# Optimization experiments

Hardware: AMD Instinct MI355X
Metric: run time of the kernel (lower is better)

## Reference

```python
import jax, jax.numpy as jnp
import numpy as np
import math

B, S, F, D = 8, 2048, 1024, 1024
NEG = -1e9


def setup_inputs() -> dict:
    key = jax.random.key(0)
    ks = jax.random.split(key, 5)
    x = jax.random.normal(ks[0], (B, S, F), dtype=jnp.float32)
    r_mat = jax.random.normal(ks[1], (B, S, S), dtype=jnp.float32)
    # shared causal attention mask [S, S] (1 = keep, 0 = masked)
    attn_mask = jnp.tril(jnp.ones((S, S), dtype=jnp.float32))
    # per-batch padding mask [B, 1, S]: last 128 tokens of half the batch padded
    pad = jnp.ones((B, 1, S), dtype=jnp.float32)
    pad = pad.at[B // 2:, :, S - 128:].set(0.0)
    Wq = jax.random.normal(ks[2], (F, D), dtype=jnp.float32) / math.sqrt(F)
    Wk = jax.random.normal(ks[3], (F, D), dtype=jnp.float32) / math.sqrt(F)
    Wv = jax.random.normal(ks[4], (F, D), dtype=jnp.float32) / math.sqrt(F)
    return {"x": x, "r_mat": r_mat, "attn_mask": attn_mask, "pad_mask": pad,
            "Wq": Wq, "Wk": Wk, "Wv": Wv}


def reference(x, r_mat, attn_mask, pad_mask, Wq, Wk, Wv):
    scale = math.sqrt(x.shape[-1])  # original scales by sqrt(features)
    q = jnp.einsum('bsf,fd->bsd', x, Wq)
    k = jnp.einsum('bsf,fd->bsd', x, Wk)
    v = jnp.einsum('bsf,fd->bsd', x, Wv)
    scores = jnp.einsum('bsd,btd->bst', q, k) / scale  # [B, S, S]
    keep = (pad_mask != 0.0) & (attn_mask[None] != 0.0)  # [B, S, S] broadcast
    r = jnp.where(keep, r_mat, NEG)
    r = jax.nn.softmax(r, axis=-1)
    scores = jnp.where(keep, scores + r, NEG)
    prob = jax.nn.softmax(scores, axis=-1)
    return jnp.einsum('bst,btd->bsd', prob, v)
```

## Files before the change

kernel.cpp:

```cpp
#include <hip/hip_runtime.h>
#include <hip/hip_bf16.h>

#define B_ 8
#define S_ 2048
#define F_ 1024
#define D_ 1024
#define TRI_ 136
#define TELEM_ 16384

typedef unsigned short u16;
typedef float f32x4 __attribute__((ext_vector_type(4)));
typedef __bf16 bf16x8 __attribute__((ext_vector_type(8)));
typedef unsigned short u16x8 __attribute__((ext_vector_type(8)));

__device__ __forceinline__ u16 f2bf(float f) {
  union { float f; unsigned u; } v; v.f = f;
  unsigned r = v.u + 0x7fff + ((v.u >> 16) & 1);
  return (u16)(r >> 16);
}
__device__ __forceinline__ float bf2f(u16 b) {
  union { unsigned u; float f; } v; v.u = ((unsigned)b) << 16;
  return v.f;
}

__device__ __forceinline__ void stage16(const u16* g, u16* l) {
  __builtin_amdgcn_global_load_lds(
      (const __attribute__((address_space(1))) void*)g,
      (__attribute__((address_space(3))) void*)l, 16, 0, 0);
}

__device__ __forceinline__ int xcd_swz(int f, int n) {
  int per = n >> 3;
  return (f & 7) * per + (f >> 3);
}


__global__ __launch_bounds__(256) void prep(const float* __restrict__ x,
                                            const float* __restrict__ Wq,
                                            const float* __restrict__ Wk,
                                            const float* __restrict__ Wv,
                                            u16* __restrict__ xb,
                                            u16* __restrict__ Wt) {
  __shared__ float tile[32][33];
  if (blockIdx.x < 2048) {
    int n4 = (B_ * S_ * F_) / 4;
    for (int i = blockIdx.x * 256 + threadIdx.x; i < n4; i += 2048 * 256) {
      float4 v = ((const float4*)x)[i];
      ushort4 o;
      o.x = f2bf(v.x); o.y = f2bf(v.y); o.z = f2bf(v.z); o.w = f2bf(v.w);
      ((ushort4*)xb)[i] = o;
    }
  } else {
    int f = blockIdx.x - 2048;
    int z = f >> 10;
    int f2 = f & 1023;
    int f0 = (f2 >> 5) * 32, d0 = (f2 & 31) * 32;
    const float* W = (z == 0) ? Wq : ((z == 1) ? Wk : Wv);
    int tx = threadIdx.x & 31, ty = threadIdx.x >> 5;
    for (int i = 0; i < 4; i++)
      tile[ty + i * 8][tx] = W[(size_t)(f0 + ty + i * 8) * D_ + d0 + tx];
    __syncthreads();
    u16* o = Wt + (size_t)z * D_ * F_;
    for (int i = 0; i < 4; i++)
      o[(size_t)(d0 + ty + i * 8) * F_ + f0 + tx] = f2bf(tile[tx][ty + i * 8]);
  }
}

__global__ __launch_bounds__(256) void er_pass(const float* __restrict__ r,
                                               const float* __restrict__ pm,
                                               u16* __restrict__ er,
                                               float* __restrict__ rowsum) {
  int row = blockIdx.x;
  int b = row >> 11, s = row & 2047;
  if (threadIdx.x == 0) rowsum[row] = 0.f;
  const float4* rp = (const float4*)(r + (size_t)row * S_);
  const float4* pp = (const float4*)(pm + (size_t)b * S_);
  int nk = (s >> 2) + 1;
  int nw = ((s >> 7) + 1) << 5;
  float4 ev[8];
  float acc = 0.f;
  #pragma unroll
  for (int it = 0; it < 8; it++) {
    int i = threadIdx.x + it * 256;
    if (i < nk) {
      float4 rv = rp[i], pv = pp[i];
      int t0 = i << 2;
      float4 e;
      #pragma unroll
      for (int j = 0; j < 4; j++) {
        bool keep = (t0 + j <= s) && ((&pv.x)[j] != 0.f);
        (&e.x)[j] = keep ? __expf((&rv.x)[j] - 16.f) : 0.f;
        acc += (&e.x)[j];
      }
      ev[it] = e;
    }
  }
  for (int off = 1; off < 64; off <<= 1) acc += __shfl_xor(acc, off);
  __shared__ float wsum[4];
  int lane = threadIdx.x & 63, w = threadIdx.x >> 6;
  if (lane == 0) wsum[w] = acc;
  __syncthreads();
  float invr = 1.f / (wsum[0] + wsum[1] + wsum[2] + wsum[3]);
  int c = s >> 7, rin = s & 127;
  u16* tb = er + (size_t)(b * TRI_ + c * (c + 1) / 2) * TELEM_ + rin * 128;
  #pragma unroll
  for (int it = 0; it < 8; it++) {
    int i = threadIdx.x + it * 256;
    if (i < nw) {
      int t0 = i << 2;
      float4 pv = pp[i];
      ushort4 o;
      #pragma unroll
      for (int j = 0; j < 4; j++) {
        bool keep = (t0 + j <= s) && ((&pv.x)[j] != 0.f);
        float val = keep ? (&ev[it].x)[j] * invr : -1e9f;
        (&o.x)[j] = f2bf(val);
      }
      *(ushort4*)(tb + (size_t)(t0 >> 7) * TELEM_ + (t0 & 127)) = o;
    }
  }
}

__global__ __launch_bounds__(256) void r_rowsum(const float* __restrict__ r,
                                                const float* __restrict__ pm,
                                                float* __restrict__ rs) {
  int row = blockIdx.x;
  int b = row >> 11, s = row & 2047;
  const float4* rp = (const float4*)(r + (size_t)row * S_);
  const float4* pp = (const float4*)(pm + (size_t)b * S_);
  int nv = (s >> 2) + 1;
  float acc = 0.f;
  for (int i = threadIdx.x; i < nv; i += 256) {
    float4 rv = rp[i];
    float4 pv = pp[i];
    int t0 = i << 2;
    #pragma unroll
    for (int j = 0; j < 4; j++) {
      int t = t0 + j;
      if (t <= s && (&pv.x)[j] != 0.f) acc += __expf((&rv.x)[j] - 16.f);
    }
  }
  for (int off = 1; off < 64; off <<= 1) acc += __shfl_xor(acc, off);
  __shared__ float wsum[4];
  int lane = threadIdx.x & 63, w = threadIdx.x >> 6;
  if (lane == 0) wsum[w] = acc;
  __syncthreads();
  if (threadIdx.x == 0) rs[row] = wsum[0] + wsum[1] + wsum[2] + wsum[3];
}


__device__ __forceinline__ bf16x8 readfrag(const u16* lds, int row, int ks, int hi) {
  int c = ((ks << 6) + (hi << 4)) ^ ((row & 7) << 4);
  return *(const bf16x8*)((const char*)lds + row * 128 + c);
}

#define SYNC_POINT()                                                             \
  __builtin_amdgcn_sched_barrier(0);                                             \
  __builtin_amdgcn_s_barrier();                                                  \
  __builtin_amdgcn_sched_barrier(0);


__device__ __forceinline__ void stageA(const u16* __restrict__ src, int ld, int h,
                                       u16* ldsA, int w, int l) {
  int base = ((w >> 2) * 128) + h * 64 + ((w & 3) * 16);
  int r = l >> 3, ch = (l & 7) ^ (l >> 3);
  #pragma unroll
  for (int i = 0; i < 2; i++) {
    int row = base + i * 8;
    stage16(src + (size_t)(row + r) * ld + ch * 8, ldsA + row * 64);
  }
}
__device__ __forceinline__ void stageB(const u16* __restrict__ src, int ld, int h,
                                       u16* ldsB, int w, int l) {
  int base = h * 128 + w * 16;
  int r = l >> 3, ch = (l & 7) ^ (l >> 3);
  #pragma unroll
  for (int i = 0; i < 2; i++) {
    int row = base + i * 8;
    stage16(src + (size_t)(row + r) * ld + ch * 8, ldsB + row * 64);
  }
}

#define MFMAQ(AF, KB, MB)                                                        \
  __builtin_amdgcn_s_setprio(1);                                                 \
  _Pragma("unroll")                                                              \
  for (int m = 0; m < 4; m++)                                                    \
    _Pragma("unroll")                                                            \
    for (int n = 0; n < 4; n++)                                                  \
      acc[(MB) + m][n] = __builtin_amdgcn_mfma_f32_16x16x32_bf16(                \
          AF[m], bfr[(KB) + n], acc[(MB) + m][n], 0, 0, 0);                      \
  __builtin_amdgcn_s_setprio(0);

__device__ __forceinline__ void gemm256(const u16* __restrict__ A, int lda,
                                        const u16* __restrict__ B, int ldb,
                                        int nT, u16* lds, f32x4 acc[8][4]) {
  const int t = threadIdx.x, w = t >> 6, l = t & 63;
  const int wr = w >> 2, wc = w & 3;
  u16* A0 = lds;           u16* B0 = lds + 16384;
  u16* A1 = lds + 32768;   u16* B1 = lds + 49152;

  #pragma unroll
  for (int m = 0; m < 8; m++)
    #pragma unroll
    for (int n = 0; n < 4; n++)
      #pragma unroll
      for (int j = 0; j < 4; j++) acc[m][n][j] = 0.f;

  stageB(B, ldb, 0, B0, w, l);
  stageB(B, ldb, 1, B0, w, l);
  stageA(A, lda, 0, A0, w, l);
  stageA(A, lda, 1, A0, w, l);
  if (nT > 1) stageA(A + 64, lda, 0, A1, w, l);
  asm volatile("s_waitcnt vmcnt(4)" ::: "memory");
  SYNC_POINT()

  const int arow = wr * 128 + (l & 15), hi = l >> 4;
  const int brow = wc * 64 + (l & 15);

  for (int kt = 0; kt < nT; kt++) {
    u16* cA = (kt & 1) ? A1 : A0;
    u16* cB = (kt & 1) ? B1 : B0;
    u16* nA = (kt & 1) ? A0 : A1;
    u16* nB = (kt & 1) ? B0 : B1;
    const u16* An1 = A + (size_t)(kt + 1) * 64;
    const u16* Bn1 = B + (size_t)(kt + 1) * 64;
    const u16* An2 = A + (size_t)(kt + 2) * 64;
    const bool has1 = (kt + 1 < nT), has2 = (kt + 2 < nT);
    bf16x8 af0[4], af1[4], bfr[8];

    #pragma unroll
    for (int m = 0; m < 4; m++) af0[m] = readfrag(cA, arow + m * 16, 0, hi);
    #pragma unroll
    for (int n = 0; n < 4; n++) bfr[n] = readfrag(cB, brow + n * 16, 0, hi);
    #pragma unroll
    for (int m = 0; m < 4; m++) af1[m] = readfrag(cA, arow + m * 16, 1, hi);
    #pragma unroll
    for (int n = 0; n < 4; n++) bfr[4 + n] = readfrag(cB, brow + n * 16, 1, hi);
    if (has1) stageB(Bn1, ldb, 0, nB, w, l);
    MFMAQ(af0, 0, 0)

    if (has1) {
      stageB(Bn1, ldb, 1, nB, w, l);
      asm volatile("s_waitcnt vmcnt(4)" ::: "memory");
    } else {
      asm volatile("s_waitcnt vmcnt(0)" ::: "memory");
    }
    SYNC_POINT()
    MFMAQ(af1, 4, 0)

    #pragma unroll
    for (int m = 0; m < 4; m++) af0[m] = readfrag(cA, arow + 64 + m * 16, 0, hi);
    #pragma unroll
    for (int m = 0; m < 4; m++) af1[m] = readfrag(cA, arow + 64 + m * 16, 1, hi);
    if (has2) stageA(An2, lda, 0, cA, w, l);
    MFMAQ(af0, 0, 4)

    if (has1) stageA(An1, lda, 1, nA, w, l);
    if (has1 && has2)  { asm volatile("s_waitcnt vmcnt(4)" ::: "memory"); }
    else if (has1)     { asm volatile("s_waitcnt vmcnt(2)" ::: "memory"); }
    else               { asm volatile("s_waitcnt vmcnt(0)" ::: "memory"); }
    SYNC_POINT()
    MFMAQ(af1, 4, 4)
  }
}

__device__ __forceinline__ void store256_bf16(f32x4 acc[8][4], u16* smem,
                                              u16* dst, int ld) {
  int t = threadIdx.x, w = t >> 6, l = t & 63;
  int wr = w >> 2, wc = w & 3;
  #pragma unroll
  for (int q = 0; q < 4; q++) {
    __syncthreads();
    if (wr == (q >> 1)) {
      int mb = (q & 1) * 4;
      #pragma unroll
      for (int mm = 0; mm < 4; mm++)
        #pragma unroll
        for (int j = 0; j < 4; j++) {
          int row = mm * 16 + (l >> 4) * 4 + j;
          #pragma unroll
          for (int n = 0; n < 4; n++)
            smem[row * 264 + wc * 64 + n * 16 + (l & 15)] = f2bf(acc[mb + mm][n][j]);
        }
    }
    __syncthreads();
    #pragma unroll
    for (int i = 0; i < 4; i++) {
      int idx = i * 512 + t;
      int row = idx >> 5, ch = idx & 31;
      *(u16x8*)(dst + (size_t)(q * 64 + row) * ld + ch * 8) =
          *(const u16x8*)(smem + row * 264 + ch * 8);
    }
  }
}

__global__ __launch_bounds__(512, 2) void gemm_qkv(
    const u16* __restrict__ xb, const u16* __restrict__ Wt,
    u16* __restrict__ qb, u16* __restrict__ kb, u16* __restrict__ vT) {
  __shared__ __align__(16) u16 lds[65536];
  int z = blockIdx.z;
  f32x4 acc[8][4];
  if (z < 2) {
    int m0 = blockIdx.x * 256, n0 = blockIdx.y * 256;
    gemm256(xb + (size_t)m0 * F_, F_,
            Wt + (size_t)z * D_ * F_ + (size_t)n0 * F_, F_, F_ / 64, lds, acc);
    store256_bf16(acc, lds, ((z == 0) ? qb : kb) + (size_t)m0 * D_ + n0, D_);
  } else {
    int d0 = blockIdx.y * 256, s0g = blockIdx.x * 256;
    gemm256(Wt + 2ULL * D_ * F_ + (size_t)d0 * F_, F_,
            xb + (size_t)s0g * F_, F_, F_ / 64, lds, acc);
    int b = s0g >> 11, s0 = s0g & 2047;
    store256_bf16(acc, lds, vT + (size_t)b * D_ * S_ + (size_t)d0 * S_ + s0, S_);
  }
}


template <int PACKA>
__device__ __forceinline__ void gemm128(const u16* __restrict__ A, int lda,
                                        const u16* __restrict__ B, int ldb,
                                        int nT, u16* lds, f32x4 acc[4][4]) {
  const int t = threadIdx.x, w = t >> 6, l = t & 63;
  const int wr = w >> 1, wc = w & 1;
  u16* A0 = lds;          u16* B0 = lds + 8192;
  u16* A1 = lds + 16384;  u16* B1 = lds + 24576;

  auto asrc = [&](int kt) -> const u16* {
    return PACKA ? A + (size_t)(kt >> 1) * TELEM_ + (kt & 1) * 64
                 : A + (size_t)kt * 64;
  };

  #pragma unroll
  for (int m = 0; m < 4; m++)
    #pragma unroll
    for (int n = 0; n < 4; n++)
      #pragma unroll
      for (int j = 0; j < 4; j++) acc[m][n][j] = 0.f;

  auto stg = [&](const u16* src, int ld, int h, u16* dst) {
    int base = h * 64 + w * 16;
    int r = l >> 3, ch = (l & 7) ^ (l >> 3);
    #pragma unroll
    for (int i = 0; i < 2; i++) {
      int row = base + i * 8;
      stage16(src + (size_t)(row + r) * ld + ch * 8, dst + row * 64);
    }
  };

  stg(asrc(0), PACKA ? 128 : lda, 0, A0);
  stg(asrc(0), PACKA ? 128 : lda, 1, A0);
  stg(B, ldb, 0, B0);
  stg(B, ldb, 1, B0);
  if (nT > 1) {
    stg(asrc(1), PACKA ? 128 : lda, 0, A1);
    stg(asrc(1), PACKA ? 128 : lda, 1, A1);
    asm volatile("s_waitcnt vmcnt(4)" ::: "memory");
  } else {
    asm volatile("s_waitcnt vmcnt(0)" ::: "memory");
  }
  SYNC_POINT()

  const int arow = wr * 64 + (l & 15), brow = wc * 64 + (l & 15), hi = l >> 4;

  for (int kt = 0; kt < nT; kt++) {
    u16* cA = (kt & 1) ? A1 : A0;
    u16* cB = (kt & 1) ? B1 : B0;
    u16* nB = (kt & 1) ? B0 : B1;
    const bool has1 = (kt + 1 < nT), has2 = (kt + 2 < nT);
    bf16x8 a0f[4], b0f[4], a1f[4], b1f[4];

    #pragma unroll
    for (int m = 0; m < 4; m++) a0f[m] = readfrag(cA, arow + m * 16, 0, hi);
    #pragma unroll
    for (int n = 0; n < 4; n++) b0f[n] = readfrag(cB, brow + n * 16, 0, hi);
    #pragma unroll
    for (int m = 0; m < 4; m++) a1f[m] = readfrag(cA, arow + m * 16, 1, hi);
    #pragma unroll
    for (int n = 0; n < 4; n++) b1f[n] = readfrag(cB, brow + n * 16, 1, hi);
    if (has1) {
      stg(B + (size_t)(kt + 1) * 64, ldb, 0, nB);
      stg(B + (size_t)(kt + 1) * 64, ldb, 1, nB);
    }
    __builtin_amdgcn_s_setprio(1);
    #pragma unroll
    for (int m = 0; m < 4; m++)
      #pragma unroll
      for (int n = 0; n < 4; n++)
        acc[m][n] = __builtin_amdgcn_mfma_f32_16x16x32_bf16(a0f[m], b0f[n], acc[m][n], 0, 0, 0);
    __builtin_amdgcn_s_setprio(0);
    asm volatile("s_waitcnt lgkmcnt(0)" ::: "memory");
    SYNC_POINT()

    if (has2) {
      stg(asrc(kt + 2), PACKA ? 128 : lda, 0, cA);
      stg(asrc(kt + 2), PACKA ? 128 : lda, 1, cA);
    }
    __builtin_amdgcn_s_setprio(1);
    #pragma unroll
    for (int m = 0; m < 4; m++)
      #pragma unroll
      for (int n = 0; n < 4; n++)
        acc[m][n] = __builtin_amdgcn_mfma_f32_16x16x32_bf16(a1f[m], b1f[n], acc[m][n], 0, 0, 0);
    __builtin_amdgcn_s_setprio(0);
    if (has2)      { asm volatile("s_waitcnt vmcnt(4)" ::: "memory"); }
    else if (has1) { asm volatile("s_waitcnt vmcnt(0)" ::: "memory"); }
    SYNC_POINT()
  }
}

__device__ __forceinline__ void tri_decode(int x, int& mt, int& nt) {
  mt = (int)((sqrtf(8.f * x + 1.f) - 1.f) * 0.5f);
  while ((mt + 1) * (mt + 2) / 2 <= x) mt++;
  while (mt * (mt + 1) / 2 > x) mt--;
  nt = x - mt * (mt + 1) / 2;
}

__global__ __launch_bounds__(512, 2) void attn_scores_er(
    const u16* __restrict__ qb, const u16* __restrict__ kb,
    const u16* __restrict__ er, u16* __restrict__ P,
    float* __restrict__ rowsum) {
  __shared__ __align__(16) u16 lds[65536];
  int f = xcd_swz(blockIdx.x + 36 * blockIdx.y, 288);
  int x = f % 36, b = f / 36;
  int MT, NT; tri_decode(x, MT, NT);
  int m0 = MT * 256, n0 = NT * 256;
  f32x4 acc[8][4];
  gemm256(qb + ((size_t)b * S_ + m0) * D_, D_,
          kb + ((size_t)b * S_ + n0) * D_, D_, D_ / 64, lds, acc);
  int t = threadIdx.x, w = t >> 6, l = t & 63;
  int wr = w >> 2, wc = w & 3;
  float* fs = (float*)lds;
  const u16* erb = er + (size_t)b * TRI_ * TELEM_;
  u16* Pb = P + (size_t)b * TRI_ * TELEM_;
  #pragma unroll
  for (int q = 0; q < 4; q++) {
    __syncthreads();
    if (wr == (q >> 1)) {
      int mb = (q & 1) * 4;
      #pragma unroll
      for (int mm = 0; mm < 4; mm++)
        #pragma unroll
        for (int j = 0; j < 4; j++) {
          int row = mm * 16 + (l >> 4) * 4 + j;
          #pragma unroll
          for (int n = 0; n < 4; n++)
            fs[row * 260 + wc * 64 + n * 16 + (l & 15)] = acc[mb + mm][n][j];
        }
    }
    __syncthreads();
    int row = t >> 3, cg = t & 7;
    int rin256 = q * 64 + row;
    int mt128 = 2 * MT + (rin256 >> 7), rin128 = rin256 & 127;
    int nt128 = 2 * NT + (cg >> 2);
    bool valid = (nt128 <= mt128);
    float rsum = 0.f;
    if (valid) {
      size_t sb = (size_t)(mt128 * (mt128 + 1) / 2 + nt128) * TELEM_
                  + (size_t)rin128 * 128 + (cg & 3) * 32;
      const u16* et = erb + sb;
      u16* pt = Pb + sb;
      const float* fsc = fs + row * 260 + cg * 32;
      #pragma unroll
      for (int cc = 0; cc < 4; cc++) {
        int ch = (cg + cc) & 3;
        f32x4 q0 = *(const f32x4*)(fsc + ch * 8);
        f32x4 q1 = *(const f32x4*)(fsc + ch * 8 + 4);
        u16x8 e8 = *(const u16x8*)(et + ch * 8);
        u16x8 o;
        #pragma unroll
        for (int k = 0; k < 8; k++) {
          float qk = (k < 4) ? q0[k] : q1[k - 4];
          float e = __expf(fmaf(qk, 0.03125f, bf2f(e8[k]) - 16.f));
          u16 pb = f2bf(e); o[k] = pb; rsum += bf2f(pb);
        }
        *(u16x8*)(pt + ch * 8) = o;
      }
    }
    rsum += __shfl_xor(rsum, 1);
    rsum += __shfl_xor(rsum, 2);
    rsum += __shfl_xor(rsum, 4);
    if ((t & 7) == 0) atomicAdd(&rowsum[b * S_ + m0 + rin256], rsum);
  }
}

__global__ __launch_bounds__(256, 2) void attn_scores_rm(
    const u16* __restrict__ qb, const u16* __restrict__ kb,
    const float* __restrict__ r_mat, const float* __restrict__ pm,
    const float* __restrict__ rs_r, u16* __restrict__ P,
    float* __restrict__ rowsum) {
  __shared__ __align__(16) u16 lds[32768];
  int f = xcd_swz(blockIdx.x + 136 * blockIdx.y, 1088);
  int x = f % 136, b = f / 136;
  int mt, nt; tri_decode(x, mt, nt);
  int m0 = mt * 128, n0 = nt * 128;
  f32x4 acc[4][4];
  gemm128<0>(qb + ((size_t)b * S_ + m0) * D_, D_,
             kb + ((size_t)b * S_ + n0) * D_, D_, D_ / 64, lds, acc);
  int t = threadIdx.x, w = t >> 6, l = t & 63;
  int wr = w >> 1, wc = w & 1;
  float* fs = (float*)lds;
  const float* rb = r_mat + (size_t)b * S_ * S_;
  const float* pmp = pm + (size_t)b * S_ + n0;
  size_t tbase = (size_t)(b * TRI_ + mt * (mt + 1) / 2 + nt) * TELEM_;
  #pragma unroll
  for (int h = 0; h < 2; h++) {
    __syncthreads();
    if (wr == h) {
      #pragma unroll
      for (int m = 0; m < 4; m++)
        #pragma unroll
        for (int j = 0; j < 4; j++) {
          int row = m * 16 + (l >> 4) * 4 + j;
          #pragma unroll
          for (int n = 0; n < 4; n++)
            fs[row * 132 + wc * 64 + n * 16 + (l & 15)] = acc[m][n][j];
        }
    }
    __syncthreads();
    int row = t >> 2, cg = t & 3;
    int srow = m0 + h * 64 + row;
    float invr = 1.f / rs_r[b * S_ + srow];
    const float* rrow = rb + (size_t)srow * S_ + n0 + cg * 32;
    u16* pt = P + tbase + (size_t)(h * 64 + row) * 128 + cg * 32;
    const float* fsc = fs + row * 132 + cg * 32;
    float rsum = 0.f;
    #pragma unroll
    for (int cc = 0; cc < 4; cc++) {
      int ch = (cg + cc) & 3;
      f32x4 q0 = *(const f32x4*)(fsc + ch * 8);
      f32x4 q1 = *(const f32x4*)(fsc + ch * 8 + 4);
      f32x4 r0 = *(const f32x4*)(rrow + ch * 8);
      f32x4 r1 = *(const f32x4*)(rrow + ch * 8 + 4);
      f32x4 p0 = *(const f32x4*)(pmp + cg * 32 + ch * 8);
      f32x4 p1 = *(const f32x4*)(pmp + cg * 32 + ch * 8 + 4);
      u16x8 o;
      #pragma unroll
      for (int k = 0; k < 8; k++) {
        int tc = n0 + cg * 32 + ch * 8 + k;
        float rv = (k < 4) ? r0[k] : r1[k - 4];
        float pmv = (k < 4) ? p0[k] : p1[k - 4];
        float qk = (k < 4) ? q0[k] : q1[k - 4];
        bool keep = (tc <= srow) && (pmv != 0.f);
        float rsm = __expf(rv - 16.f) * invr;
        float e = keep ? __expf(fmaf(qk, 0.03125f, rsm - 16.f)) : 0.f;
        u16 pb = f2bf(e); o[k] = pb; rsum += bf2f(pb);
      }
      *(u16x8*)(pt + ch * 8) = o;
    }
    rsum += __shfl_xor(rsum, 1);
    rsum += __shfl_xor(rsum, 2);
    if ((t & 3) == 0) atomicAdd(&rowsum[b * S_ + srow], rsum);
  }
}

__global__ __launch_bounds__(256, 2) void attn_pv(
    const u16* __restrict__ P, const u16* __restrict__ vT,
    const float* __restrict__ rowsum, float* __restrict__ out) {
  __shared__ __align__(16) u16 lds[32768];
  int f = xcd_swz(blockIdx.x + 8 * blockIdx.y + 64 * blockIdx.z, 512);
  int mtp = f & 7, dt = (f >> 3) & 7, b = f >> 6;
  for (int hf = 0; hf < 2; hf++) {
    int mt = hf ? mtp : (15 - mtp);
    int m0 = mt * 128, n0 = dt * 128;
    int nT = 2 * (mt + 1);
    f32x4 acc[4][4];
    gemm128<1>(P + (size_t)(b * TRI_ + mt * (mt + 1) / 2) * TELEM_, 128,
               vT + ((size_t)b * D_ + n0) * S_, S_, nT, lds, acc);
    int t = threadIdx.x, w = t >> 6, l = t & 63;
    int wr = w >> 1, wc = w & 1;
    float* fs = (float*)lds;
    #pragma unroll
    for (int h = 0; h < 2; h++) {
      __syncthreads();
      if (wr == h) {
        #pragma unroll
        for (int m = 0; m < 4; m++)
          #pragma unroll
          for (int j = 0; j < 4; j++) {
            int row = m * 16 + (l >> 4) * 4 + j;
            float inv = 1.f / rowsum[b * S_ + m0 + h * 64 + row];
            #pragma unroll
            for (int n = 0; n < 4; n++)
              fs[row * 132 + wc * 64 + n * 16 + (l & 15)] = acc[m][n][j] * inv;
          }
      }
      __syncthreads();
      #pragma unroll
      for (int i = 0; i < 8; i++) {
        int idx = i * 256 + t;
        int row = idx >> 5, c4 = (idx & 31) << 2;
        *(float4*)(out + ((size_t)b * S_ + m0 + h * 64 + row) * D_ + n0 + c4) =
            *(const float4*)(fs + row * 132 + c4);
      }
    }
    __syncthreads();
  }
}

extern "C" void kernel_launch(void* const* d_in, const int* in_sizes, int n_in,
                              void* d_out, int out_size, void* d_ws, size_t ws_size,
                              hipStream_t stream) {
  const float* x     = (const float*)d_in[0];
  const float* r_mat = (const float*)d_in[1];
  const float* pm    = (const float*)d_in[3];
  const float* Wq    = (const float*)d_in[4];
  const float* Wk    = (const float*)d_in[5];
  const float* Wv    = (const float*)d_in[6];
  float* out = (float*)d_out;
  char* ws = (char*)d_ws;

  const size_t PK = (size_t)B_ * TRI_ * TELEM_ * 2;
  u16*   qb     = (u16*)(ws + 0);
  u16*   kb     = (u16*)(ws + 33554432ULL);
  u16*   vT     = (u16*)(ws + 67108864ULL);
  float* rowsum = (float*)(ws + 100663296ULL);
  float* rs_r   = (float*)(ws + 100728832ULL);
  u16*   xb     = (u16*)(ws + 100794368ULL);
  u16*   Wt     = (u16*)(ws + 134348800ULL);
  u16*   er     = (u16*)(ws + 100794368ULL);
  bool use_er   = ws_size >= 100794368ULL + 2 * PK;
  u16*   P      = use_er ? (u16*)(ws + 100794368ULL + PK)
                         : (u16*)(ws + 100794368ULL);

  prep<<<dim3(5120), dim3(256), 0, stream>>>(x, Wq, Wk, Wv, xb, Wt);
  if (!use_er)
    r_rowsum<<<dim3(B_ * S_), dim3(256), 0, stream>>>(r_mat, pm, rs_r);
  gemm_qkv<<<dim3(64, 4, 3), dim3(512), 0, stream>>>(xb, Wt, qb, kb, vT);
  if (use_er) {
    er_pass<<<dim3(B_ * S_), dim3(256), 0, stream>>>(r_mat, pm, er, rowsum);
    attn_scores_er<<<dim3(36, 8), dim3(512), 0, stream>>>(qb, kb, er, P, rowsum);
  } else {
    hipMemsetAsync(rowsum, 0, B_ * S_ * sizeof(float), stream);
    attn_scores_rm<<<dim3(136, 8), dim3(256), 0, stream>>>(qb, kb, r_mat, pm, rs_r, P, rowsum);
  }
  attn_pv<<<dim3(8, 8, 8), dim3(256), 0, stream>>>(P, vT, rowsum, out);
}
```

Measured before the change: 268.0 us.

## Fuse r-matrix softmax pass into QKV GEMM launch as extra grid slice

Adds a fourth z-slice to the QKV GEMM grid whose blocks compute the masked exp-normalized r tiles (er) and zero rowsum, so this memory-bound pass overlaps with the compute-bound GEMM. When the workspace is large enough, er is placed past Wt and P aliases er in place, and the separate er_pass launch is dropped. This costs an extra launch slot per block group and relies on the attn_scores kernel writing P over er safely in place.

```diff
diff --git a/kernel.cpp b/kernel.cpp
--- a/kernel.cpp
+++ b/kernel.cpp
@@ -66,6 +66,61 @@
   }
 }
 
+__device__ __forceinline__ void er_rows(const float* __restrict__ r,
+                                        const float* __restrict__ pm,
+                                        u16* __restrict__ er,
+                                        float* __restrict__ rowsum,
+                                        int rowbase) {
+  int wid = threadIdx.x >> 6, lane = threadIdx.x & 63;
+  for (int i = 0; i < 8; i++) {
+    int row = rowbase + wid + i * 8;
+    int b = row >> 11, s = row & 2047;
+    if (lane == 0) rowsum[row] = 0.f;
+    const float4* rp = (const float4*)(r + (size_t)row * S_);
+    const float4* pp = (const float4*)(pm + (size_t)b * S_);
+    int nk = (s >> 2) + 1;
+    int nw = ((s >> 7) + 1) << 5;
+    float4 ev[8];
+    float acc = 0.f;
+    #pragma unroll
+    for (int it = 0; it < 8; it++) {
+      int q = lane + it * 64;
+      if (q < nk) {
+        float4 rv = rp[q], pv = pp[q];
+        int t0 = q << 2;
+        float4 e;
+        #pragma unroll
+        for (int j = 0; j < 4; j++) {
+          bool keep = (t0 + j <= s) && ((&pv.x)[j] != 0.f);
+          (&e.x)[j] = keep ? __expf((&rv.x)[j] - 16.f) : 0.f;
+          acc += (&e.x)[j];
+        }
+        ev[it] = e;
+      }
+    }
+    for (int off = 1; off < 64; off <<= 1) acc += __shfl_xor(acc, off);
+    float invr = 1.f / acc;
+    int c = s >> 7, rin = s & 127;
+    u16* tb = er + (size_t)(b * TRI_ + c * (c + 1) / 2) * TELEM_ + rin * 128;
+    #pragma unroll
+    for (int it = 0; it < 8; it++) {
+      int q = lane + it * 64;
+      if (q < nw) {
+        int t0 = q << 2;
+        float4 pv = pp[q];
+        ushort4 o;
+        #pragma unroll
+        for (int j = 0; j < 4; j++) {
+          bool keep = (t0 + j <= s) && ((&pv.x)[j] != 0.f);
+          float val = keep ? (&ev[it].x)[j] * invr : -1e9f;
+          (&o.x)[j] = f2bf(val);
+        }
+        *(ushort4*)(tb + (size_t)(t0 >> 7) * TELEM_ + (t0 & 127)) = o;
+      }
+    }
+  }
+}
+
 __global__ __launch_bounds__(256) void er_pass(const float* __restrict__ r,
                                                const float* __restrict__ pm,
                                                u16* __restrict__ er,
@@ -296,9 +351,15 @@
 
 __global__ __launch_bounds__(512, 2) void gemm_qkv(
     const u16* __restrict__ xb, const u16* __restrict__ Wt,
-    u16* __restrict__ qb, u16* __restrict__ kb, u16* __restrict__ vT) {
+    u16* __restrict__ qb, u16* __restrict__ kb, u16* __restrict__ vT,
+    const float* __restrict__ r_mat, const float* __restrict__ pm,
+    u16* __restrict__ er, float* __restrict__ rowsum) {
   __shared__ __align__(16) u16 lds[65536];
   int z = blockIdx.z;
+  if (z == 3) {
+    er_rows(r_mat, pm, er, rowsum, (blockIdx.x + 64 * blockIdx.y) * 64);
+    return;
+  }
   f32x4 acc[8][4];
   if (z < 2) {
     int m0 = blockIdx.x * 256, n0 = blockIdx.y * 256;
@@ -616,17 +677,22 @@
   float* rs_r   = (float*)(ws + 100728832ULL);
   u16*   xb     = (u16*)(ws + 100794368ULL);
   u16*   Wt     = (u16*)(ws + 134348800ULL);
-  u16*   er     = (u16*)(ws + 100794368ULL);
-  bool use_er   = ws_size >= 100794368ULL + 2 * PK;
-  u16*   P      = use_er ? (u16*)(ws + 100794368ULL + PK)
-                         : (u16*)(ws + 100794368ULL);
+  bool   big    = ws_size >= 140640256ULL + PK;
+  bool   use_er = big || ws_size >= 100794368ULL + 2 * PK;
+  u16*   er     = big ? (u16*)(ws + 140640256ULL)
+                      : (u16*)(ws + 100794368ULL);
+  u16*   P      = big ? er
+                      : (use_er ? (u16*)(ws + 100794368ULL + PK)
+                                : (u16*)(ws + 100794368ULL));
 
   prep<<<dim3(5120), dim3(256), 0, stream>>>(x, Wq, Wk, Wv, xb, Wt);
   if (!use_er)
     r_rowsum<<<dim3(B_ * S_), dim3(256), 0, stream>>>(r_mat, pm, rs_r);
-  gemm_qkv<<<dim3(64, 4, 3), dim3(512), 0, stream>>>(xb, Wt, qb, kb, vT);
+  gemm_qkv<<<dim3(64, 4, big ? 4 : 3), dim3(512), 0, stream>>>(
+      xb, Wt, qb, kb, vT, r_mat, pm, er, rowsum);
   if (use_er) {
-    er_pass<<<dim3(B_ * S_), dim3(256), 0, stream>>>(r_mat, pm, er, rowsum);
+    if (!big)
+      er_pass<<<dim3(B_ * S_), dim3(256), 0, stream>>>(r_mat, pm, er, rowsum);
     attn_scores_er<<<dim3(36, 8), dim3(512), 0, stream>>>(qb, kb, er, P, rowsum);
   } else {
     hipMemsetAsync(rowsum, 0, B_ * S_ * sizeof(float), stream);
```

Result: slower. 322.0 us (+20.1%).
